# Optimization experiments

Hardware: AMD Instinct MI355X
Metric: run time of the kernel (lower is better)

The kernel has to match this reference:

```python
import jax, jax.numpy as jnp
import numpy as np

N_NODES = 50000
N_EDGES = 800000
IN_F = 128
OUT_F = 32
HEADS = 4
EDGE_F = 32  # must equal OUT_F for the original module's shapes to broadcast


def setup_inputs() -> dict:
    key = jax.random.key(0)
    k1, k2, k3, k4, k5, k6, k7 = jax.random.split(key, 7)
    h = jax.random.normal(k1, (N_NODES, IN_F), dtype=jnp.float32)
    edge_indices = jax.random.randint(k2, (2, N_EDGES), 0, N_NODES, dtype=jnp.int32)
    edge_attr = jax.random.normal(k3, (N_EDGES, EDGE_F), dtype=jnp.float32)
    # learned parameters (xavier-ish scaling)
    W = jax.random.normal(k4, (IN_F, HEADS * OUT_F), dtype=jnp.float32) * (1.0 / np.sqrt(IN_F))
    a = jax.random.normal(k5, (HEADS, 2 * OUT_F + EDGE_F), dtype=jnp.float32) * 0.1
    eW = jax.random.normal(k6, (EDGE_F, HEADS * OUT_F), dtype=jnp.float32) * (1.0 / np.sqrt(EDGE_F))
    eb = jnp.zeros((HEADS * OUT_F,), dtype=jnp.float32)
    return {"h": h, "edge_indices": edge_indices, "edge_attr": edge_attr,
            "W": W, "a": a, "eW": eW, "eb": eb}


def reference(h, edge_indices, edge_attr, W, a, eW, eb):
    N = h.shape[0]
    H = a.shape[0]
    F = W.shape[1] // H
    row, col = edge_indices[0], edge_indices[1]

    # node / edge projections
    ht = (h @ W).reshape(N, H, F)                       # [N,H,F]
    et = (edge_attr @ eW + eb).reshape(-1, H, F)        # [E,H,F]

    # split attention vector; avoids materializing the [E,H,3F] concat
    a_i, a_j, a_e = a[:, :F], a[:, F:2 * F], a[:, 2 * F:]
    alpha_i = jnp.einsum('nhf,hf->nh', ht, a_i)         # [N,H]
    alpha_j = jnp.einsum('nhf,hf->nh', ht, a_j)         # [N,H]
    e = alpha_i[row] + alpha_j[col] + jnp.einsum('ehf,hf->eh', et, a_e)  # [E,H]
    e = jax.nn.leaky_relu(e, negative_slope=0.2)

    # scatter-softmax over edges grouped by destination (row), global-max stabilized
    e_exp = jnp.exp(e - jnp.max(e))                     # matches torch exp(e - e.max())
    denom = jax.ops.segment_sum(e_exp, row, num_segments=N)  # [N,H]
    att = e_exp / (denom[row] + 1e-8)                   # [E,H]

    # weighted scatter-add aggregation
    hj = ht[col]                                        # [E,H,F]
    h_out = jax.ops.segment_sum(att[:, :, None] * hj, row, num_segments=N)  # [N,H,F]
    h_out = h_out.reshape(N, H * F)                     # concat=True
    h_out = jax.nn.elu(h_out)                           # dropout=0 (eval)
    return h_out, att
```

## Files before the change

### kernel.cpp

```cpp
#include <hip/hip_runtime.h>
#include <hip/hip_bf16.h>
#include <hip/hip_fp16.h>

#define N_NODES 50000
#define N_EDGES 800000
#define IN_F 128
#define OUT_F 32
#define HEADS 4
#define EDGE_F 32
#define HF 128
#define SB 256
#define NBLK ((N_NODES + SB - 1) / SB)

typedef __attribute__((ext_vector_type(8))) short short8_t;
typedef __attribute__((ext_vector_type(4))) float f32x4;

__device__ __forceinline__ unsigned short f2bf(float x) {
    unsigned int u = __float_as_uint(x);
    unsigned int r = (u + 0x7FFF + ((u >> 16) & 1)) >> 16;
    return (unsigned short)r;
}
__device__ __forceinline__ float bf2f(unsigned short b) {
    return __uint_as_float(((unsigned int)b) << 16);
}

__global__ void prep_kernel(const float* __restrict__ eW, const float* __restrict__ eb,
                            const float* __restrict__ a,
                            float* __restrict__ w_eff, float* __restrict__ b_eff) {
    int t = threadIdx.x;
    if (t < 128) {
        int k = t >> 2, h = t & 3;
        float s = 0.f;
        #pragma unroll
        for (int f = 0; f < EDGE_F; ++f)
            s = fmaf(eW[k * HF + h * OUT_F + f], a[h * 96 + 2 * OUT_F + f], s);
        w_eff[k * 4 + h] = s;
    } else if (t < 132) {
        int h = t - 128;
        float s = 0.f;
        #pragma unroll
        for (int f = 0; f < EDGE_F; ++f)
            s = fmaf(eb[h * OUT_F + f], a[h * 96 + 2 * OUT_F + f], s);
        b_eff[h] = s;
    }
}

__global__ __launch_bounds__(256) void prepW_kernel(const float* __restrict__ W,
                                                    unsigned short* __restrict__ W_T) {
    int g = blockIdx.x * 256 + threadIdx.x;
    int n = g >> 4, c = g & 15;
    unsigned short w8[8];
    #pragma unroll
    for (int q = 0; q < 8; ++q)
        w8[q] = f2bf(W[(size_t)(8 * c + q) * 128 + n]);
    *(uint4*)&W_T[n * 128 + ((c ^ (n & 7)) << 3)] = *(uint4*)w8;
}

__global__ __launch_bounds__(256) void node_kernel(
        const float* __restrict__ h, const unsigned short* __restrict__ W_T,
        const float* __restrict__ a,
        __hip_bfloat16* __restrict__ ht_bf,
        float* __restrict__ alpha_i, float* __restrict__ alpha_j) {
    __shared__ __align__(16) unsigned short Wl[128 * 128];
    __shared__ __align__(16) unsigned short Hhi[64 * 128];
    __shared__ __align__(16) unsigned short Hlo[64 * 128];
    int t = threadIdx.x;
    int lane = t & 63, wave = t >> 6;
    int nb = blockIdx.x * 64;
    {
        const uint4* src = (const uint4*)W_T;
        uint4* dst = (uint4*)Wl;
        #pragma unroll
        for (int u = 0; u < 8; ++u) dst[t + u * 256] = src[t + u * 256];
    }
    #pragma unroll
    for (int u = 0; u < 8; ++u) {
        int f = u * 256 + t;
        int row = f >> 5, q = f & 31;
        int gn = nb + row; if (gn > N_NODES - 1) gn = N_NODES - 1;
        float4 v = ((const float4*)h)[(size_t)gn * 32 + q];
        unsigned short hi[4], lo[4];
        #pragma unroll
        for (int x = 0; x < 4; ++x) {
            float xv = (&v.x)[x];
            unsigned short hb = f2bf(xv);
            hi[x] = hb;
            lo[x] = f2bf(xv - bf2f(hb));
        }
        int c = q >> 1, half = q & 1;
        int off = row * 128 + ((c ^ (row & 7)) << 3) + half * 4;
        *(uint2*)&Hhi[off] = *(uint2*)hi;
        *(uint2*)&Hlo[off] = *(uint2*)lo;
    }
    __syncthreads();
    int n0 = nb + wave * 16;
    if (n0 >= N_NODES) return;
    int r = lane & 15, g = lane >> 4;
    short8_t ahi[4], alo[4];
    #pragma unroll
    for (int k = 0; k < 4; ++k) {
        int c = k * 4 + g;
        int off = (wave * 16 + r) * 128 + ((c ^ (r & 7)) << 3);
        ahi[k] = *(const short8_t*)&Hhi[off];
        alo[k] = *(const short8_t*)&Hlo[off];
    }
    f32x4 acc[8];
    #pragma unroll
    for (int i = 0; i < 8; ++i) acc[i] = (f32x4){0.f, 0.f, 0.f, 0.f};
    #pragma unroll
    for (int tt = 0; tt < 8; ++tt) {
        int n = tt * 16 + r;
        #pragma unroll
        for (int k = 0; k < 4; ++k) {
            int c = k * 4 + g;
            short8_t b = *(const short8_t*)&Wl[n * 128 + ((c ^ (n & 7)) << 3)];
            acc[tt] = __builtin_amdgcn_mfma_f32_16x16x32_bf16(ahi[k], b, acc[tt], 0, 0, 0);
            acc[tt] = __builtin_amdgcn_mfma_f32_16x16x32_bf16(alo[k], b, acc[tt], 0, 0, 0);
        }
    }
    #pragma unroll
    for (int tt = 0; tt < 8; ++tt)
        #pragma unroll
        for (int reg = 0; reg < 4; ++reg) {
            int rowg = n0 + 4 * g + reg;
            ((unsigned short*)ht_bf)[(size_t)rowg * 128 + tt * 16 + r] = f2bf(acc[tt][reg]);
        }
    float pi[4][4], pj[4][4];
    #pragma unroll
    for (int hh = 0; hh < 4; ++hh) {
        float ai0 = a[hh * 96 + r],      ai1 = a[hh * 96 + 16 + r];
        float aj0 = a[hh * 96 + 32 + r], aj1 = a[hh * 96 + 48 + r];
        #pragma unroll
        for (int reg = 0; reg < 4; ++reg) {
            float v0 = acc[2 * hh][reg], v1 = acc[2 * hh + 1][reg];
            pi[hh][reg] = fmaf(v0, ai0, v1 * ai1);
            pj[hh][reg] = fmaf(v0, aj0, v1 * aj1);
        }
    }
    #pragma unroll
    for (int hh = 0; hh < 4; ++hh)
        #pragma unroll
        for (int reg = 0; reg < 4; ++reg) {
            float vi = pi[hh][reg], vj = pj[hh][reg];
            #pragma unroll
            for (int s = 1; s < 16; s <<= 1) {
                vi += __shfl_xor(vi, s, 64);
                vj += __shfl_xor(vj, s, 64);
            }
            pi[hh][reg] = vi; pj[hh][reg] = vj;
        }
    if (r == 0) {
        #pragma unroll
        for (int hh = 0; hh < 4; ++hh)
            #pragma unroll
            for (int reg = 0; reg < 4; ++reg) {
                int rowg = n0 + 4 * g + reg;
                alpha_i[rowg * 4 + hh] = pi[hh][reg];
                alpha_j[rowg * 4 + hh] = pj[hh][reg];
            }
    }
}

__global__ __launch_bounds__(256) void count_kernel(const int* __restrict__ row,
                                                    int* __restrict__ deg,
                                                    int* __restrict__ rank) {
    int t = blockIdx.x * 256 + threadIdx.x;
    if (t < N_EDGES / 4) {
        int4 r4 = ((const int4*)row)[t];
        int4 k4;
        k4.x = atomicAdd(&deg[r4.x], 1);
        k4.y = atomicAdd(&deg[r4.y], 1);
        k4.z = atomicAdd(&deg[r4.z], 1);
        k4.w = atomicAdd(&deg[r4.w], 1);
        ((int4*)rank)[t] = k4;
    }
}

__device__ __forceinline__ int block_incl_scan(int v, int lane, int wid, int* wsum) {
    int x = v;
    #pragma unroll
    for (int s = 1; s < 64; s <<= 1) {
        int y = __shfl_up(x, s, 64);
        if (lane >= s) x += y;
    }
    if (lane == 63) wsum[wid] = x;
    __syncthreads();
    int add = 0;
    #pragma unroll
    for (int w = 0; w < 4; ++w) add += (w < wid) ? wsum[w] : 0;
    return x + add;
}

__global__ __launch_bounds__(SB) void scan1_kernel(const int* __restrict__ deg,
                                                   int* __restrict__ row_off,
                                                   int* __restrict__ blk_sums) {
    __shared__ int wsum[4];
    int i = blockIdx.x * SB + threadIdx.x;
    int v = (i < N_NODES) ? deg[i] : 0;
    int incl = block_incl_scan(v, threadIdx.x & 63, threadIdx.x >> 6, wsum);
    if (i < N_NODES) row_off[i] = incl - v;
    if (threadIdx.x == SB - 1) blk_sums[blockIdx.x] = incl;
}

__global__ __launch_bounds__(SB) void scan2_kernel(int* __restrict__ blk_sums,
                                                   int* __restrict__ blk_off,
                                                   int* __restrict__ row_off) {
    __shared__ int wsum[4];
    int t = threadIdx.x;
    int v = (t < NBLK) ? blk_sums[t] : 0;
    int incl = block_incl_scan(v, t & 63, t >> 6, wsum);
    if (t < NBLK) blk_off[t] = incl - v;
    if (t == SB - 1) row_off[N_NODES] = incl;
}

__global__ __launch_bounds__(SB) void scan3_kernel(const int* __restrict__ blk_off,
                                                   int* __restrict__ row_off) {
    int i = blockIdx.x * SB + threadIdx.x;
    if (i < N_NODES)
        row_off[i] += blk_off[blockIdx.x];
}

__global__ __launch_bounds__(256) void edge_kernel(
        const int* __restrict__ row, const int* __restrict__ col,
        const float* __restrict__ ea,
        const float* __restrict__ w_eff, const float* __restrict__ b_eff,
        const float* __restrict__ alpha_i, const float* __restrict__ alpha_j,
        const int* __restrict__ row_off, const int* __restrict__ rank,
        uint4* __restrict__ rec) {
    __shared__ __align__(16) float eas[256 * 36];
    __shared__ float wsd[128];
    __shared__ float bs[4];
    int t = threadIdx.x;
    if (t < 128) wsd[t] = w_eff[t];
    if (t < 4) bs[t] = b_eff[t];
    int e0 = blockIdx.x * 256;
    {
        const float4* src = (const float4*)ea + (size_t)e0 * 8;
        #pragma unroll
        for (int u = 0; u < 8; ++u) {
            int f = u * 256 + t;
            int el = f >> 3, j = f & 7;
            *(float4*)&eas[el * 36 + 4 * j] = src[f];
        }
    }
    __syncthreads();
    int e = e0 + t;
    float4 ev[8];
    #pragma unroll
    for (int i = 0; i < 8; ++i) ev[i] = *(const float4*)&eas[t * 36 + 4 * i];
    int r = row[e], c = col[e];
    int rk = rank[e];
    float4 ai = *(const float4*)(alpha_i + (size_t)r * 4);
    float4 aj = *(const float4*)(alpha_j + (size_t)c * 4);
    float s0 = bs[0], s1 = bs[1], s2 = bs[2], s3 = bs[3];
    #pragma unroll
    for (int i = 0; i < 8; ++i) {
        #pragma unroll
        for (int kk = 0; kk < 4; ++kk) {
            float x = (&ev[i].x)[kk];
            float4 w4 = *(const float4*)&wsd[(i * 4 + kk) * 4];
            s0 = fmaf(x, w4.x, s0);
            s1 = fmaf(x, w4.y, s1);
            s2 = fmaf(x, w4.z, s2);
            s3 = fmaf(x, w4.w, s3);
        }
    }
    float e0v = s0 + ai.x + aj.x;
    float e1v = s1 + ai.y + aj.y;
    float e2v = s2 + ai.z + aj.z;
    float e3v = s3 + ai.w + aj.w;
    e0v = e0v > 0.f ? e0v : 0.2f * e0v;
    e1v = e1v > 0.f ? e1v : 0.2f * e1v;
    e2v = e2v > 0.f ? e2v : 0.2f * e2v;
    e3v = e3v > 0.f ? e3v : 0.2f * e3v;
    __half2 p01 = __floats2half2_rn(__expf(e0v), __expf(e1v));
    __half2 p23 = __floats2half2_rn(__expf(e2v), __expf(e3v));
    uint4 out;
    out.x = *reinterpret_cast<unsigned int*>(&p01);
    out.y = *reinterpret_cast<unsigned int*>(&p23);
    out.z = (unsigned int)c;
    out.w = (unsigned int)e;
    int pos = row_off[r] + rk;
    rec[pos] = out;
}

__global__ __launch_bounds__(256) void agg_kernel(
        const int* __restrict__ row_off, const uint4* __restrict__ rec,
        const __hip_bfloat16* __restrict__ ht_bf,
        float* __restrict__ hout, float* __restrict__ att) {
    int wave = threadIdx.x >> 6;
    int lane = threadIdx.x & 63;
    int n = blockIdx.x * 4 + wave;
    if (n >= N_NODES) return;
    int beg = row_off[n], end = row_off[n + 1];
    int h2 = lane >> 4;
    int sh = (h2 & 1) * 16;
    float2 acc0 = {0.f, 0.f}, acc1 = {0.f, 0.f};
    float den0 = 0.f, den1 = 0.f;
    int p = beg;
    for (; p + 1 < end; p += 2) {
        uint4 rA = rec[p];
        uint4 rB = rec[p + 1];
        unsigned int wA = (h2 & 2) ? rA.y : rA.x;
        unsigned int wB = (h2 & 2) ? rB.y : rB.x;
        float exA = __half2float(__ushort_as_half((unsigned short)(wA >> sh)));
        float exB = __half2float(__ushort_as_half((unsigned short)(wB >> sh)));
        int cA = (int)rA.z;
        int cB = (int)rB.z;
        float2 hvA = __bfloat1622float2(
            *(const __hip_bfloat162*)(ht_bf + (size_t)cA * HF + 2 * lane));
        float2 hvB = __bfloat1622float2(
            *(const __hip_bfloat162*)(ht_bf + (size_t)cB * HF + 2 * lane));
        acc0.x = fmaf(exA, hvA.x, acc0.x); acc0.y = fmaf(exA, hvA.y, acc0.y);
        acc1.x = fmaf(exB, hvB.x, acc1.x); acc1.y = fmaf(exB, hvB.y, acc1.y);
        den0 += exA; den1 += exB;
    }
    if (p < end) {
        uint4 rA = rec[p];
        unsigned int wA = (h2 & 2) ? rA.y : rA.x;
        float exA = __half2float(__ushort_as_half((unsigned short)(wA >> sh)));
        int cA = (int)rA.z;
        float2 hvA = __bfloat1622float2(
            *(const __hip_bfloat162*)(ht_bf + (size_t)cA * HF + 2 * lane));
        acc0.x = fmaf(exA, hvA.x, acc0.x); acc0.y = fmaf(exA, hvA.y, acc0.y);
        den0 += exA;
    }
    float den = den0 + den1;
    float rden = 1.0f / (den + 1e-8f);
    float ox = (acc0.x + acc1.x) * rden, oy = (acc0.y + acc1.y) * rden;
    ox = ox > 0.f ? ox : expm1f(ox);
    oy = oy > 0.f ? oy : expm1f(oy);
    float2 o = {ox, oy};
    ((float2*)(hout + (size_t)n * HF))[lane] = o;
    int h = lane & 3;
    float rden_h = __shfl(rden, h * 16, 64);
    for (int p0 = beg; p0 < end; p0 += 16) {
        int q = p0 + (lane >> 2);
        if (q < end) {
            uint4 rQ = rec[q];
            unsigned int w = (h & 2) ? rQ.y : rQ.x;
            float ex = __half2float(__ushort_as_half((unsigned short)(w >> ((h & 1) * 16))));
            att[(size_t)rQ.w * 4 + h] = ex * rden_h;
        }
    }
}

extern "C" void kernel_launch(void* const* d_in, const int* in_sizes, int n_in,
                              void* d_out, int out_size, void* d_ws, size_t ws_size,
                              hipStream_t stream) {
    const float* h  = (const float*)d_in[0];
    const int*   ei = (const int*)  d_in[1];
    const float* ea = (const float*)d_in[2];
    const float* W  = (const float*)d_in[3];
    const float* a  = (const float*)d_in[4];
    const float* eW = (const float*)d_in[5];
    const float* eb = (const float*)d_in[6];

    float* out  = (float*)d_out;
    float* hout = out;
    float* att  = out + (size_t)N_NODES * HF;

    char* wsb = (char*)d_ws;
    __hip_bfloat16* ht_bf = (__hip_bfloat16*)wsb;
    float* alpha_i = (float*)(wsb + (size_t)N_NODES * HF * 2);
    float* alpha_j = alpha_i + N_NODES * HEADS;
    float* w_eff   = alpha_j + N_NODES * HEADS;
    float* b_eff   = w_eff + 128;
    unsigned short* W_T = (unsigned short*)(b_eff + 4);
    int*   deg     = (int*)(W_T + 128 * 128);
    int*   row_off = deg + N_NODES;
    int*   blk_sums= row_off + N_NODES + 1;
    int*   blk_off = blk_sums + NBLK;
    int*   rank    = (int*)((((uintptr_t)(blk_off + NBLK)) + 15) & ~(uintptr_t)15);
    uint4* rec     = (uint4*)((((uintptr_t)(rank + N_EDGES)) + 15) & ~(uintptr_t)15);

    const int* row = ei;
    const int* col = ei + N_EDGES;

    hipMemsetAsync(deg, 0, (size_t)N_NODES * sizeof(int), stream);

    prep_kernel<<<1, 160, 0, stream>>>(eW, eb, a, w_eff, b_eff);
    prepW_kernel<<<8, 256, 0, stream>>>(W, W_T);
    node_kernel<<<(N_NODES + 63) / 64, 256, 0, stream>>>(h, W_T, a, ht_bf, alpha_i, alpha_j);
    count_kernel<<<(N_EDGES / 4 + 255) / 256, 256, 0, stream>>>(row, deg, rank);
    scan1_kernel<<<NBLK, SB, 0, stream>>>(deg, row_off, blk_sums);
    scan2_kernel<<<1, SB, 0, stream>>>(blk_sums, blk_off, row_off);
    scan3_kernel<<<NBLK, SB, 0, stream>>>(blk_off, row_off);
    edge_kernel<<<N_EDGES / 256, 256, 0, stream>>>(row, col, ea, w_eff, b_eff,
                                                   alpha_i, alpha_j, row_off, rank, rec);
    agg_kernel<<<(N_NODES + 3) / 4, 256, 0, stream>>>(row_off, rec, ht_bf, hout, att);
}
```

Before: 337.2 us.

## Write unnormalized attention coalesced in edge kernel, normalize in separate pass

The edge kernel now writes fp32 exp values directly into the att output in edge order (coalesced float4), and the aggregation kernel only stores per-node reciprocal denominators. A new norm kernel then scales att by the per-row reciprocal, replacing the scattered per-edge att writes from the aggregation kernel. The aggregation loop is also unrolled to four records per iteration to raise memory-level parallelism on the gathers. This costs an extra kernel launch plus a full read-modify-write of att and a gather of rden_buf per edge.

```diff
diff --git a/kernel.cpp b/kernel.cpp
--- a/kernel.cpp
+++ b/kernel.cpp
@@ -226,7 +226,7 @@
         const float* __restrict__ w_eff, const float* __restrict__ b_eff,
         const float* __restrict__ alpha_i, const float* __restrict__ alpha_j,
         const int* __restrict__ row_off, const int* __restrict__ rank,
-        uint4* __restrict__ rec) {
+        uint4* __restrict__ rec, float* __restrict__ att_ex) {
     __shared__ __align__(16) float eas[256 * 36];
     __shared__ float wsd[128];
     __shared__ float bs[4];
@@ -273,13 +273,15 @@
     e1v = e1v > 0.f ? e1v : 0.2f * e1v;
     e2v = e2v > 0.f ? e2v : 0.2f * e2v;
     e3v = e3v > 0.f ? e3v : 0.2f * e3v;
-    __half2 p01 = __floats2half2_rn(__expf(e0v), __expf(e1v));
-    __half2 p23 = __floats2half2_rn(__expf(e2v), __expf(e3v));
+    float x0 = __expf(e0v), x1 = __expf(e1v), x2 = __expf(e2v), x3 = __expf(e3v);
+    ((float4*)att_ex)[e] = make_float4(x0, x1, x2, x3);
+    __half2 p01 = __floats2half2_rn(x0, x1);
+    __half2 p23 = __floats2half2_rn(x2, x3);
     uint4 out;
     out.x = *reinterpret_cast<unsigned int*>(&p01);
     out.y = *reinterpret_cast<unsigned int*>(&p23);
     out.z = (unsigned int)c;
-    out.w = (unsigned int)e;
+    out.w = 0u;
     int pos = row_off[r] + rk;
     rec[pos] = out;
 }
@@ -287,7 +289,7 @@
 __global__ __launch_bounds__(256) void agg_kernel(
         const int* __restrict__ row_off, const uint4* __restrict__ rec,
         const __hip_bfloat16* __restrict__ ht_bf,
-        float* __restrict__ hout, float* __restrict__ att) {
+        float* __restrict__ hout, float* __restrict__ rden_buf) {
     int wave = threadIdx.x >> 6;
     int lane = threadIdx.x & 63;
     int n = blockIdx.x * 4 + wave;
@@ -298,30 +300,39 @@
     float2 acc0 = {0.f, 0.f}, acc1 = {0.f, 0.f};
     float den0 = 0.f, den1 = 0.f;
     int p = beg;
-    for (; p + 1 < end; p += 2) {
+    for (; p + 3 < end; p += 4) {
         uint4 rA = rec[p];
         uint4 rB = rec[p + 1];
+        uint4 rC = rec[p + 2];
+        uint4 rD = rec[p + 3];
         unsigned int wA = (h2 & 2) ? rA.y : rA.x;
         unsigned int wB = (h2 & 2) ? rB.y : rB.x;
+        unsigned int wC = (h2 & 2) ? rC.y : rC.x;
+        unsigned int wD = (h2 & 2) ? rD.y : rD.x;
         float exA = __half2float(__ushort_as_half((unsigned short)(wA >> sh)));
         float exB = __half2float(__ushort_as_half((unsigned short)(wB >> sh)));
-        int cA = (int)rA.z;
-        int cB = (int)rB.z;
+        float exC = __half2float(__ushort_as_half((unsigned short)(wC >> sh)));
+        float exD = __half2float(__ushort_as_half((unsigned short)(wD >> sh)));
         float2 hvA = __bfloat1622float2(
-            *(const __hip_bfloat162*)(ht_bf + (size_t)cA * HF + 2 * lane));
+            *(const __hip_bfloat162*)(ht_bf + (size_t)rA.z * HF + 2 * lane));
         float2 hvB = __bfloat1622float2(
-            *(const __hip_bfloat162*)(ht_bf + (size_t)cB * HF + 2 * lane));
+            *(const __hip_bfloat162*)(ht_bf + (size_t)rB.z * HF + 2 * lane));
+        float2 hvC = __bfloat1622float2(
+            *(const __hip_bfloat162*)(ht_bf + (size_t)rC.z * HF + 2 * lane));
+        float2 hvD = __bfloat1622float2(
+            *(const __hip_bfloat162*)(ht_bf + (size_t)rD.z * HF + 2 * lane));
         acc0.x = fmaf(exA, hvA.x, acc0.x); acc0.y = fmaf(exA, hvA.y, acc0.y);
         acc1.x = fmaf(exB, hvB.x, acc1.x); acc1.y = fmaf(exB, hvB.y, acc1.y);
-        den0 += exA; den1 += exB;
-    }
-    if (p < end) {
+        acc0.x = fmaf(exC, hvC.x, acc0.x); acc0.y = fmaf(exC, hvC.y, acc0.y);
+        acc1.x = fmaf(exD, hvD.x, acc1.x); acc1.y = fmaf(exD, hvD.y, acc1.y);
+        den0 += exA + exC; den1 += exB + exD;
+    }
+    for (; p < end; ++p) {
         uint4 rA = rec[p];
         unsigned int wA = (h2 & 2) ? rA.y : rA.x;
         float exA = __half2float(__ushort_as_half((unsigned short)(wA >> sh)));
-        int cA = (int)rA.z;
         float2 hvA = __bfloat1622float2(
-            *(const __hip_bfloat162*)(ht_bf + (size_t)cA * HF + 2 * lane));
+            *(const __hip_bfloat162*)(ht_bf + (size_t)rA.z * HF + 2 * lane));
         acc0.x = fmaf(exA, hvA.x, acc0.x); acc0.y = fmaf(exA, hvA.y, acc0.y);
         den0 += exA;
     }
@@ -332,17 +343,19 @@
     oy = oy > 0.f ? oy : expm1f(oy);
     float2 o = {ox, oy};
     ((float2*)(hout + (size_t)n * HF))[lane] = o;
-    int h = lane & 3;
-    float rden_h = __shfl(rden, h * 16, 64);
-    for (int p0 = beg; p0 < end; p0 += 16) {
-        int q = p0 + (lane >> 2);
-        if (q < end) {
-            uint4 rQ = rec[q];
-            unsigned int w = (h & 2) ? rQ.y : rQ.x;
-            float ex = __half2float(__ushort_as_half((unsigned short)(w >> ((h & 1) * 16))));
-            att[(size_t)rQ.w * 4 + h] = ex * rden_h;
-        }
-    }
+    if ((lane & 15) == 0)
+        rden_buf[n * 4 + h2] = rden;
+}
+
+__global__ __launch_bounds__(256) void norm_kernel(const int* __restrict__ row,
+                                                   const float* __restrict__ rden_buf,
+                                                   float* __restrict__ att) {
+    int e = blockIdx.x * 256 + threadIdx.x;
+    float4 ex = ((const float4*)att)[e];
+    int r = row[e];
+    float4 rd = *(const float4*)(rden_buf + (size_t)r * 4);
+    ex.x *= rd.x; ex.y *= rd.y; ex.z *= rd.z; ex.w *= rd.w;
+    ((float4*)att)[e] = ex;
 }
 
 extern "C" void kernel_launch(void* const* d_in, const int* in_sizes, int n_in,
@@ -373,6 +386,7 @@
     int*   blk_off = blk_sums + NBLK;
     int*   rank    = (int*)((((uintptr_t)(blk_off + NBLK)) + 15) & ~(uintptr_t)15);
     uint4* rec     = (uint4*)((((uintptr_t)(rank + N_EDGES)) + 15) & ~(uintptr_t)15);
+    float* rden_buf= (float*)(rec + N_EDGES);
 
     const int* row = ei;
     const int* col = ei + N_EDGES;
@@ -387,6 +401,8 @@
     scan2_kernel<<<1, SB, 0, stream>>>(blk_sums, blk_off, row_off);
     scan3_kernel<<<NBLK, SB, 0, stream>>>(blk_off, row_off);
     edge_kernel<<<N_EDGES / 256, 256, 0, stream>>>(row, col, ea, w_eff, b_eff,
-                                                   alpha_i, alpha_j, row_off, rank, rec);
-    agg_kernel<<<(N_NODES + 3) / 4, 256, 0, stream>>>(row_off, rec, ht_bf, hout, att);
-}
+                                                   alpha_i, alpha_j, row_off, rank,
+                                                   rec, att);
+    agg_kernel<<<(N_NODES + 3) / 4, 256, 0, stream>>>(row_off, rec, ht_bf, hout, rden_buf);
+    norm_kernel<<<N_EDGES / 256, 256, 0, stream>>>(row, rden_buf, att);
+}
```

New measurement: 328.2 us. -2.7%, faster.
